# Optimization experiments

Measured on AMD Instinct MI355X. Metric: run time of the kernel, lower is better.

The kernel has to match this reference:

```python
import jax, jax.numpy as jnp
import numpy as np

H, D = 16, 1024
HD = D // H  # 64

def setup_inputs() -> dict:
    key = jax.random.key(0)
    ks = jax.random.split(key, 11)
    B, S = 2, 2048
    s_in = 1.0 / np.sqrt(D)
    return {
        "V": jax.random.normal(ks[0], (B, S, D), jnp.float32),
        "K": jax.random.normal(ks[1], (B, S, D), jnp.float32),
        "Q": jax.random.normal(ks[2], (B, S, D), jnp.float32),
        # stacked per-head Linear weights, torch layout [out,in] -> [H, HD, D]
        "Wv": jax.random.normal(ks[3], (H, HD, D), jnp.float32) * s_in,
        "bv": jnp.zeros((H, HD), jnp.float32),
        "Wk": jax.random.normal(ks[4], (H, HD, D), jnp.float32) * s_in,
        "bk": jnp.zeros((H, HD), jnp.float32),
        "Wq": jax.random.normal(ks[5], (H, HD, D), jnp.float32) * s_in,
        "bq": jnp.zeros((H, HD), jnp.float32),
        "Wo": jax.random.normal(ks[6], (D, D), jnp.float32) * s_in,
        "bo": jnp.zeros((D,), jnp.float32),
    }

def reference(V, K, Q, Wv, bv, Wk, bk, Wq, bq, Wo, bo):
    scale = HD ** (-0.5)
    # per-head projections fused into one batched GEMM: [B,S,D] x [H,HD,D] -> [B,H,S,HD]
    q = jnp.einsum('bsd,hed->bhse', Q, Wq) + bq[None, :, None, :]
    k = jnp.einsum('bsd,hed->bhse', K, Wk) + bk[None, :, None, :]
    v = jnp.einsum('bsd,hed->bhse', V, Wv) + bv[None, :, None, :]
    # scaled dot-product attention
    scores = jnp.einsum('bhqe,bhke->bhqk', q, k) * scale  # [B,H,S,S]
    p = jax.nn.softmax(scores, axis=-1)
    att = jnp.einsum('bhqk,bhke->bhqe', p, v)  # [B,H,S,HD]
    # concat heads (head 0 first, matching the torch cat order) then output proj
    B, _, S, _ = att.shape
    cat = jnp.transpose(att, (0, 2, 1, 3)).reshape(B, S, H * HD)
    return cat @ Wo.T + bo
```

## Files before the change

### kernel.cpp

```cpp
#include <hip/hip_runtime.h>
#include <cstdint>
#include <cstddef>

typedef __bf16 bf16_t;
typedef bf16_t bf16x8 __attribute__((ext_vector_type(8)));
typedef bf16_t bf16x4 __attribute__((ext_vector_type(4)));
typedef float f32x4 __attribute__((ext_vector_type(4)));
typedef float f32x2 __attribute__((ext_vector_type(2)));

__device__ __forceinline__ void gl_lds16(const void* g, void* l) {
  __builtin_amdgcn_global_load_lds(
      (const __attribute__((address_space(1))) void*)g,
      (__attribute__((address_space(3))) void*)l, 16, 0, 0);
}

__device__ __forceinline__ f32x4 mfma16(bf16x8 a, bf16x8 b, f32x4 c) {
  return __builtin_amdgcn_mfma_f32_16x16x32_bf16(a, b, c, 0, 0, 0);
}

__device__ __forceinline__ float exp2_fast(float x) {
  float r;
  asm("v_exp_f32 %0, %1" : "=v"(r) : "v"(x));
  return r;
}

#define SCHED_FENCE() __builtin_amdgcn_sched_barrier(0)
#define WAIT_VM0()   do { asm volatile("s_waitcnt vmcnt(0)");   SCHED_FENCE(); } while (0)
#define WAIT_LGKM0() do { asm volatile("s_waitcnt lgkmcnt(0)"); SCHED_FENCE(); } while (0)
#define RAW_BAR()    do { __builtin_amdgcn_s_barrier();         SCHED_FENCE(); } while (0)

struct CvtArgs { const float* src[7]; bf16_t* dst[7]; };

__global__ __launch_bounds__(256) void convert_all(CvtArgs a) {
  unsigned g = blockIdx.x * 256u + threadIdx.x;
  unsigned seg, off;
  if (g < 524288u) {
    seg = g >> 17; off = g & 131071u;
  } else {
    unsigned h = g - 524288u;
    seg = 4u + (h >> 19); off = h & 524287u;
  }
  const float4* s = (const float4*)a.src[seg] + (size_t)off * 2;
  float4 x0 = s[0], x1 = s[1];
  bf16x8 o;
  o[0] = (bf16_t)x0.x; o[1] = (bf16_t)x0.y; o[2] = (bf16_t)x0.z; o[3] = (bf16_t)x0.w;
  o[4] = (bf16_t)x1.x; o[5] = (bf16_t)x1.y; o[6] = (bf16_t)x1.z; o[7] = (bf16_t)x1.w;
  *(bf16x8*)(a.dst[seg] + (size_t)off * 8) = o;
}

__device__ __forceinline__ void stage128(const bf16_t* src, bf16_t* dst, int t, int w) {
  #pragma unroll
  for (int i = 0; i < 4; i++) {
    int g = t + i * 256;
    int r = g >> 3, pc = g & 7;
    int lc = pc ^ (r & 7);
    gl_lds16(src + (size_t)r * 1024 + lc * 8, dst + i * 2048 + w * 512);
  }
}
__device__ __forceinline__ void stage64(const bf16_t* src, bf16_t* dst, int t, int w) {
  #pragma unroll
  for (int i = 0; i < 2; i++) {
    int g = t + i * 256;
    int r = g >> 3, pc = g & 7;
    int lc = pc ^ (r & 7);
    gl_lds16(src + (size_t)r * 1024 + lc * 8, dst + i * 2048 + w * 512);
  }
}

struct ProjArgs {
  const bf16_t* A[3]; const bf16_t* W[3]; const float* bias[3];
  bf16_t* out[3]; float scale[3];
};

__global__ __launch_bounds__(256, 2) void gemm_proj(ProjArgs p) {
  __shared__ __attribute__((aligned(16))) unsigned char smem[65536];
  const int z = blockIdx.z;
  const bf16_t* A = p.A[z] + (size_t)blockIdx.x * 128 * 1024;
  const bf16_t* W = p.W[z] + (size_t)blockIdx.y * 128 * 1024;

  const int t = threadIdx.x;
  const int w = t >> 6, l = t & 63;
  const int lq = l >> 4, lr = l & 15;
  const int mq = w & 1, nq = w >> 1;

  f32x4 acc[4][4];
  f32x4 zero = {0.f, 0.f, 0.f, 0.f};
  #pragma unroll
  for (int i = 0; i < 4; i++)
    #pragma unroll
    for (int j = 0; j < 4; j++) acc[i][j] = zero;

  stage128(A, (bf16_t*)smem, t, w);
  stage128(W, (bf16_t*)(smem + 16384), t, w);
  WAIT_VM0();
  RAW_BAR();

  for (int step = 0; step < 16; ++step) {
    const int cur = step & 1;
    bf16_t* as = (bf16_t*)(smem + cur * 32768);
    bf16_t* bs = (bf16_t*)(smem + cur * 32768 + 16384);
    if (step < 15) {
      bf16_t* an = (bf16_t*)(smem + (cur ^ 1) * 32768);
      stage128(A + (step + 1) * 64, an, t, w);
      stage128(W + (step + 1) * 64, an + 8192, t, w);
    }
    SCHED_FENCE();
    #pragma unroll
    for (int kk = 0; kk < 2; kk++) {
      bf16x8 af[4], bfr[4];
      #pragma unroll
      for (int i = 0; i < 4; i++) {
        int R = mq * 64 + i * 16 + lr;
        int ch = (kk * 4 + lq) ^ (R & 7);
        af[i] = *(const bf16x8*)(as + R * 64 + ch * 8);
      }
      #pragma unroll
      for (int j = 0; j < 4; j++) {
        int R = nq * 64 + j * 16 + lr;
        int ch = (kk * 4 + lq) ^ (R & 7);
        bfr[j] = *(const bf16x8*)(bs + R * 64 + ch * 8);
      }
      __builtin_amdgcn_s_setprio(1);
      #pragma unroll
      for (int i = 0; i < 4; i++)
        #pragma unroll
        for (int j = 0; j < 4; j++)
          acc[i][j] = mfma16(af[i], bfr[j], acc[i][j]);
      __builtin_amdgcn_s_setprio(0);
    }
    WAIT_VM0();
    RAW_BAR();
  }

  const float* bias = p.bias[z];
  const float scale = p.scale[z];
  __syncthreads();
  bf16_t* ts = (bf16_t*)smem;
  #pragma unroll
  for (int i = 0; i < 4; i++) {
    #pragma unroll
    for (int j = 0; j < 4; j++) {
      int nl = nq * 64 + j * 16 + lr;
      float bz = bias[blockIdx.y * 128 + nl];
      #pragma unroll
      for (int r = 0; r < 4; r++) {
        int ml = mq * 64 + i * 16 + lq * 4 + r;
        bf16_t val = (bf16_t)((acc[i][j][r] + bz) * scale);
        if (z == 0) {
          int mlp = (ml & 96) | (((ml >> 2) & 3) << 3) | (((ml >> 4) & 1) << 2) | (ml & 3);
          ts[nl * 136 + mlp] = val;
        } else {
          ts[ml * 136 + nl] = val;
        }
      }
    }
  }
  __syncthreads();
  bf16_t* out = p.out[z];
  const int b = blockIdx.x >> 4, sbase = (blockIdx.x & 15) * 128;
  if (z == 0) {
    #pragma unroll
    for (int ii = 0; ii < 8; ii++) {
      int idx = t * 8 + ii * 2048;
      int rr = idx >> 7, cc = idx & 127;
      int n = blockIdx.y * 128 + rr;
      int h = n >> 6, e = n & 63;
      bf16x8 vq = *(const bf16x8*)(ts + rr * 136 + cc);
      *(bf16x8*)(out + ((size_t)(b * 16 + h) * 64 + e) * 2048 + sbase + cc) = vq;
    }
  } else {
    #pragma unroll
    for (int ii = 0; ii < 8; ii++) {
      int idx = t * 8 + ii * 2048;
      int rr = idx >> 7, cc = idx & 127;
      int n = blockIdx.y * 128 + cc;
      int h = n >> 6, e = n & 63;
      bf16x8 vq = *(const bf16x8*)(ts + rr * 136 + cc);
      *(bf16x8*)(out + ((size_t)(b * 16 + h) * 2048 + sbase + rr) * 64 + e) = vq;
    }
  }
}

__global__ __launch_bounds__(256, 4) void attn(
    const bf16_t* __restrict__ qw, const bf16_t* __restrict__ kw,
    const bf16_t* __restrict__ vtw, bf16_t* __restrict__ att)
{
  __shared__ __attribute__((aligned(16))) unsigned char smem[32768];
  bf16_t* qe_s = (bf16_t*)(smem + 16384);
  const int bh = blockIdx.x, qt = blockIdx.y;
  const int t = threadIdx.x, w = t >> 6, l = t & 63, lq = l >> 4, lr = l & 15;

  const bf16_t* kb0 = kw + (size_t)bh * 131072;
  const bf16_t* vb0 = vtw + (size_t)bh * 131072;

  const bf16_t* qbase = qw + ((size_t)bh * 2048 + qt * 64) * 64;
  #pragma unroll
  for (int i = 0; i < 2; i++) {
    int g = t + i * 256;
    int r = g >> 3, pc = g & 7;
    int lc = pc ^ (r & 7);
    gl_lds16(qbase + (size_t)r * 64 + lc * 8, qe_s + i * 2048 + w * 512);
    gl_lds16(kb0 + (size_t)r * 64 + lc * 8, (bf16_t*)smem + i * 2048 + w * 512);
    gl_lds16(vb0 + (size_t)r * 2048 + lc * 8, (bf16_t*)(smem + 8192) + i * 2048 + w * 512);
  }
  WAIT_VM0();
  RAW_BAR();
  bf16x8 qf[2];
  #pragma unroll
  for (int kk = 0; kk < 2; kk++) {
    int R = w * 16 + lr;
    int ch = (kk * 4 + lq) ^ (R & 7);
    qf[kk] = *(const bf16x8*)(qe_s + R * 64 + ch * 8);
  }
  WAIT_LGKM0();
  RAW_BAR();

  f32x4 O[4];
  f32x4 zero = {0.f, 0.f, 0.f, 0.f};
  #pragma unroll
  for (int et = 0; et < 4; et++) O[et] = zero;
  f32x2 ls = {0.f, 0.f};
  bf16x8 vf[8];
  bf16x8 pbA[2], pbB[2];

#define ATTN_BODY(KT, CUR, PBOUT, PBIN, FIRST, DOSTAGE)                          \
  {                                                                              \
    bf16_t* ksb = (bf16_t*)(smem + (CUR) * 16384);                               \
    bf16_t* vsb = (bf16_t*)(smem + (CUR) * 16384 + 8192);                        \
    if (DOSTAGE) {                                                               \
      bf16_t* kn = (bf16_t*)(smem + ((CUR) ^ 1) * 16384);                        \
      const bf16_t* kbase = kb0 + (size_t)((KT) + 1) * 4096;                     \
      const bf16_t* vbase = vb0 + (size_t)((KT) + 1) * 64;                       \
      _Pragma("unroll")                                                          \
      for (int i = 0; i < 2; i++) {                                              \
        int g = t + i * 256;                                                     \
        int r = g >> 3, pc = g & 7;                                              \
        int lc = pc ^ (r & 7);                                                   \
        gl_lds16(kbase + (size_t)r * 64 + lc * 8, kn + i * 2048 + w * 512);      \
        gl_lds16(vbase + (size_t)r * 2048 + lc * 8, kn + 4096 + i * 2048 + w * 512); \
      }                                                                          \
    }                                                                            \
    f32x4 sc[4];                                                                 \
    _Pragma("unroll")                                                            \
    for (int j = 0; j < 4; j++) sc[j] = zero;                                    \
    __builtin_amdgcn_s_setprio(1);                                               \
    if (!(FIRST)) {                                                              \
      _Pragma("unroll")                                                          \
      for (int ks2 = 0; ks2 < 2; ks2++)                                          \
        _Pragma("unroll")                                                        \
        for (int et = 0; et < 4; et++)                                           \
          O[et] = mfma16(vf[ks2 * 4 + et], (PBIN)[ks2], O[et]);                  \
    }                                                                            \
    _Pragma("unroll")                                                            \
    for (int kk = 0; kk < 2; kk++)                                               \
      _Pragma("unroll")                                                          \
      for (int j = 0; j < 4; j++) {                                              \
        int R = j * 16 + lr;                                                     \
        int ch = (kk * 4 + lq) ^ (R & 7);                                        \
        bf16x8 kf = *(const bf16x8*)(ksb + R * 64 + ch * 8);                     \
        sc[j] = mfma16(kf, qf[kk], sc[j]);                                       \
      }                                                                          \
    __builtin_amdgcn_s_setprio(0);                                               \
    _Pragma("unroll")                                                            \
    for (int ks2 = 0; ks2 < 2; ks2++)                                            \
      _Pragma("unroll")                                                          \
      for (int et = 0; et < 4; et++) {                                           \
        int R = et * 16 + lr;                                                    \
        int ch = (ks2 * 4 + lq) ^ (R & 7);                                       \
        vf[ks2 * 4 + et] = *(const bf16x8*)(vsb + R * 64 + ch * 8);              \
      }                                                                          \
    _Pragma("unroll")                                                            \
    for (int ks2 = 0; ks2 < 2; ks2++)                                            \
      _Pragma("unroll")                                                          \
      for (int r = 0; r < 4; r++) {                                              \
        float e0 = exp2_fast(sc[2 * ks2][r]);                                    \
        float e1 = exp2_fast(sc[2 * ks2 + 1][r]);                                \
        f32x2 ee = {e0, e1};                                                     \
        ls += ee;                                                                \
        (PBOUT)[ks2][r] = (bf16_t)e0;                                            \
        (PBOUT)[ks2][4 + r] = (bf16_t)e1;                                        \
      }                                                                          \
    WAIT_LGKM0();         \
    if (DOSTAGE) WAIT_VM0();                             \
    RAW_BAR();                                                                   \
  }

  ATTN_BODY(0, 0, pbA, pbB, true, true);
  ATTN_BODY(1, 1, pbB, pbA, false, true);
  for (int kt2 = 1; kt2 < 16; ++kt2) {
    const int kt = kt2 * 2;
    ATTN_BODY(kt, 0, pbA, pbB, false, true);
    ATTN_BODY(kt + 1, 1, pbB, pbA, false, (kt2 < 15));
  }
#undef ATTN_BODY

  #pragma unroll
  for (int ks2 = 0; ks2 < 2; ks2++)
    #pragma unroll
    for (int et = 0; et < 4; et++)
      O[et] = mfma16(vf[ks2 * 4 + et], pbB[ks2], O[et]);

  float s = ls[0] + ls[1];
  s += __shfl_xor(s, 16);
  s += __shfl_xor(s, 32);
  float rinv = 1.0f / s;

  #pragma unroll
  for (int et = 0; et < 4; et++) {
    bf16x4 pv;
    #pragma unroll
    for (int r = 0; r < 4; r++) pv[r] = (bf16_t)(O[et][r] * rinv);
    *(bf16x4*)(qe_s + (w * 16 + lr) * 72 + et * 16 + lq * 4) = pv;
  }
  __syncthreads();
  const int b = bh >> 4, h = bh & 15;
  #pragma unroll
  for (int i = 0; i < 2; i++) {
    int c = t + i * 256;
    int row = c >> 3, c8 = c & 7;
    bf16x8 vv = *(const bf16x8*)(qe_s + row * 72 + c8 * 8);
    *(bf16x8*)(att + ((size_t)b * 2048 + qt * 64 + row) * 1024 + h * 64 + c8 * 8) = vv;
  }
}

__global__ __launch_bounds__(256, 3) void gemm_out(
    const bf16_t* __restrict__ A, const bf16_t* __restrict__ W,
    const float* __restrict__ bias, float* __restrict__ out)
{
  __shared__ __attribute__((aligned(16))) unsigned char smem[49152];
  const bf16_t* Ab = A + (size_t)blockIdx.x * 64 * 1024;
  const bf16_t* Wb = W + (size_t)blockIdx.y * 128 * 1024;
  const int t = threadIdx.x, w = t >> 6, l = t & 63, lq = l >> 4, lr = l & 15;
  const int mh = w & 1, nh = w >> 1;

  f32x4 acc[2][4];
  f32x4 zero = {0.f, 0.f, 0.f, 0.f};
  #pragma unroll
  for (int i = 0; i < 2; i++)
    #pragma unroll
    for (int j = 0; j < 4; j++) acc[i][j] = zero;

  stage64(Ab, (bf16_t*)smem, t, w);
  stage128(Wb, (bf16_t*)(smem + 8192), t, w);
  WAIT_VM0();
  RAW_BAR();

  for (int step = 0; step < 16; ++step) {
    const int cur = step & 1;
    bf16_t* as = (bf16_t*)(smem + cur * 24576);
    bf16_t* bs = (bf16_t*)(smem + cur * 24576 + 8192);
    if (step < 15) {
      bf16_t* an = (bf16_t*)(smem + (cur ^ 1) * 24576);
      stage64(Ab + (step + 1) * 64, an, t, w);
      stage128(Wb + (step + 1) * 64, an + 4096, t, w);
    }
    SCHED_FENCE();
    #pragma unroll
    for (int kk = 0; kk < 2; kk++) {
      bf16x8 af[2], bfr[4];
      #pragma unroll
      for (int i = 0; i < 2; i++) {
        int R = mh * 32 + i * 16 + lr;
        int ch = (kk * 4 + lq) ^ (R & 7);
        af[i] = *(const bf16x8*)(as + R * 64 + ch * 8);
      }
      #pragma unroll
      for (int j = 0; j < 4; j++) {
        int R = nh * 64 + j * 16 + lr;
        int ch = (kk * 4 + lq) ^ (R & 7);
        bfr[j] = *(const bf16x8*)(bs + R * 64 + ch * 8);
      }
      __builtin_amdgcn_s_setprio(1);
      #pragma unroll
      for (int i = 0; i < 2; i++)
        #pragma unroll
        for (int j = 0; j < 4; j++)
          acc[i][j] = mfma16(af[i], bfr[j], acc[i][j]);
      __builtin_amdgcn_s_setprio(0);
    }
    WAIT_VM0();
    RAW_BAR();
  }

  #pragma unroll
  for (int i = 0; i < 2; i++) {
    #pragma unroll
    for (int j = 0; j < 4; j++) {
      int col = blockIdx.y * 128 + nh * 64 + j * 16 + lr;
      float bz = bias[col];
      #pragma unroll
      for (int r = 0; r < 4; r++) {
        int row = blockIdx.x * 64 + mh * 32 + i * 16 + lq * 4 + r;
        out[(size_t)row * 1024 + col] = acc[i][j][r] + bz;
      }
    }
  }
}

extern "C" void kernel_launch(void* const* d_in, const int* in_sizes, int n_in,
                              void* d_out, int out_size, void* d_ws, size_t ws_size,
                              hipStream_t stream) {
  (void)in_sizes; (void)n_in; (void)out_size;
  const float* V  = (const float*)d_in[0];
  const float* Kx = (const float*)d_in[1];
  const float* Q  = (const float*)d_in[2];
  const float* Wv = (const float*)d_in[3];
  const float* bv = (const float*)d_in[4];
  const float* Wk = (const float*)d_in[5];
  const float* bk = (const float*)d_in[6];
  const float* Wq = (const float*)d_in[7];
  const float* bq = (const float*)d_in[8];
  const float* Wo = (const float*)d_in[9];
  const float* bo = (const float*)d_in[10];

  const size_t E = 1048576;
  if (ws_size < 20 * E * sizeof(bf16_t)) return;

  bf16_t* ws = (bf16_t*)d_ws;
  bf16_t* cWo   = ws;
  bf16_t* cWv   = ws + E;
  bf16_t* cWk   = ws + 2 * E;
  bf16_t* cWq   = ws + 3 * E;
  bf16_t* q_ws  = ws + 4 * E;
  bf16_t* k_ws  = ws + 8 * E;
  bf16_t* vt_ws = ws + 12 * E;
  bf16_t* att_ws= ws + 16 * E;

  bf16_t* cV = att_ws;
  bf16_t* cK = (bf16_t*)d_out;
  bf16_t* cQ = (bf16_t*)d_out + 4 * E;

  CvtArgs ca;
  ca.src[0] = Wo; ca.src[1] = Wv; ca.src[2] = Wk; ca.src[3] = Wq;
  ca.src[4] = V;  ca.src[5] = Kx; ca.src[6] = Q;
  ca.dst[0] = cWo; ca.dst[1] = cWv; ca.dst[2] = cWk; ca.dst[3] = cWq;
  ca.dst[4] = cV;  ca.dst[5] = cK;  ca.dst[6] = cQ;
  convert_all<<<8192, 256, 0, stream>>>(ca);

  ProjArgs pa;
  pa.A[0] = cV;  pa.A[1] = cK;  pa.A[2] = cQ;
  pa.W[0] = cWv; pa.W[1] = cWk; pa.W[2] = cWq;
  pa.bias[0] = bv; pa.bias[1] = bk; pa.bias[2] = bq;
  pa.out[0] = vt_ws; pa.out[1] = k_ws; pa.out[2] = q_ws;
  pa.scale[0] = 1.f; pa.scale[1] = 1.f; pa.scale[2] = 0.125f * 1.4426950408889634f;
  gemm_proj<<<dim3(32, 8, 3), 256, 0, stream>>>(pa);

  attn<<<dim3(32, 32), 256, 0, stream>>>(q_ws, k_ws, vt_ws, att_ws);

  gemm_out<<<dim3(64, 8), 256, 0, stream>>>(att_ws, cWo, bo, (float*)d_out);
}
```

Measured before the change: 205.4 us.

## Process 128 query rows per attention block to reuse K/V tiles

Each attention block now handles 128 query rows (two 16-row groups per wave) instead of 64, so each K/V tile staged in LDS feeds twice as many MFMAs. The grid is halved and launch bounds are relaxed to allow more registers for the doubled accumulators and probability fragments. This lowers global and LDS traffic per unit of work, at the cost of higher register pressure, lower occupancy and fewer blocks to spread across CUs.

```diff
diff --git a/kernel.cpp b/kernel.cpp
--- a/kernel.cpp
+++ b/kernel.cpp
@@ -181,47 +181,58 @@
   }
 }
 
-__global__ __launch_bounds__(256, 4) void attn(
+__global__ __launch_bounds__(256, 2) void attn(
     const bf16_t* __restrict__ qw, const bf16_t* __restrict__ kw,
     const bf16_t* __restrict__ vtw, bf16_t* __restrict__ att)
 {
   __shared__ __attribute__((aligned(16))) unsigned char smem[32768];
-  bf16_t* qe_s = (bf16_t*)(smem + 16384);
   const int bh = blockIdx.x, qt = blockIdx.y;
   const int t = threadIdx.x, w = t >> 6, l = t & 63, lq = l >> 4, lr = l & 15;
 
   const bf16_t* kb0 = kw + (size_t)bh * 131072;
   const bf16_t* vb0 = vtw + (size_t)bh * 131072;
-
-  const bf16_t* qbase = qw + ((size_t)bh * 2048 + qt * 64) * 64;
+  bf16_t* qstage = (bf16_t*)(smem + 16384);
+
+  const bf16_t* qbase = qw + ((size_t)bh * 2048 + qt * 128) * 64;
+  #pragma unroll
+  for (int i = 0; i < 4; i++) {
+    int g = t + i * 256;
+    int r = g >> 3, pc = g & 7;
+    int lc = pc ^ (r & 7);
+    gl_lds16(qbase + (size_t)r * 64 + lc * 8, qstage + i * 2048 + w * 512);
+  }
   #pragma unroll
   for (int i = 0; i < 2; i++) {
     int g = t + i * 256;
     int r = g >> 3, pc = g & 7;
     int lc = pc ^ (r & 7);
-    gl_lds16(qbase + (size_t)r * 64 + lc * 8, qe_s + i * 2048 + w * 512);
     gl_lds16(kb0 + (size_t)r * 64 + lc * 8, (bf16_t*)smem + i * 2048 + w * 512);
     gl_lds16(vb0 + (size_t)r * 2048 + lc * 8, (bf16_t*)(smem + 8192) + i * 2048 + w * 512);
   }
   WAIT_VM0();
   RAW_BAR();
-  bf16x8 qf[2];
-  #pragma unroll
-  for (int kk = 0; kk < 2; kk++) {
-    int R = w * 16 + lr;
-    int ch = (kk * 4 + lq) ^ (R & 7);
-    qf[kk] = *(const bf16x8*)(qe_s + R * 64 + ch * 8);
-  }
+  bf16x8 qf[2][2];
+  #pragma unroll
+  for (int gq = 0; gq < 2; gq++)
+    #pragma unroll
+    for (int kk = 0; kk < 2; kk++) {
+      int R = w * 32 + gq * 16 + lr;
+      int ch = (kk * 4 + lq) ^ (R & 7);
+      qf[gq][kk] = *(const bf16x8*)(qstage + R * 64 + ch * 8);
+    }
   WAIT_LGKM0();
   RAW_BAR();
 
-  f32x4 O[4];
+  f32x4 O[2][4];
   f32x4 zero = {0.f, 0.f, 0.f, 0.f};
   #pragma unroll
-  for (int et = 0; et < 4; et++) O[et] = zero;
-  f32x2 ls = {0.f, 0.f};
+  for (int gq = 0; gq < 2; gq++)
+    #pragma unroll
+    for (int et = 0; et < 4; et++) O[gq][et] = zero;
+  f32x2 lsv[2];
+  lsv[0] = f32x2{0.f, 0.f}; lsv[1] = f32x2{0.f, 0.f};
   bf16x8 vf[8];
-  bf16x8 pbA[2], pbB[2];
+  bf16x8 pbA[2][2], pbB[2][2];
 
 #define ATTN_BODY(KT, CUR, PBOUT, PBIN, FIRST, DOSTAGE)                          \
   {                                                                              \
@@ -240,16 +251,20 @@
         gl_lds16(vbase + (size_t)r * 2048 + lc * 8, kn + 4096 + i * 2048 + w * 512); \
       }                                                                          \
     }                                                                            \
-    f32x4 sc[4];                                                                 \
+    f32x4 sc[2][4];                                                              \
     _Pragma("unroll")                                                            \
-    for (int j = 0; j < 4; j++) sc[j] = zero;                                    \
+    for (int gq = 0; gq < 2; gq++)                                               \
+      _Pragma("unroll")                                                          \
+      for (int j = 0; j < 4; j++) sc[gq][j] = zero;                              \
     __builtin_amdgcn_s_setprio(1);                                               \
     if (!(FIRST)) {                                                              \
       _Pragma("unroll")                                                          \
       for (int ks2 = 0; ks2 < 2; ks2++)                                          \
         _Pragma("unroll")                                                        \
-        for (int et = 0; et < 4; et++)                                           \
-          O[et] = mfma16(vf[ks2 * 4 + et], (PBIN)[ks2], O[et]);                  \
+        for (int et = 0; et < 4; et++) {                                         \
+          O[0][et] = mfma16(vf[ks2 * 4 + et], (PBIN)[0][ks2], O[0][et]);         \
+          O[1][et] = mfma16(vf[ks2 * 4 + et], (PBIN)[1][ks2], O[1][et]);         \
+        }                                                                        \
     }                                                                            \
     _Pragma("unroll")                                                            \
     for (int kk = 0; kk < 2; kk++)                                               \
@@ -258,7 +273,8 @@
         int R = j * 16 + lr;                                                     \
         int ch = (kk * 4 + lq) ^ (R & 7);                                        \
         bf16x8 kf = *(const bf16x8*)(ksb + R * 64 + ch * 8);                     \
-        sc[j] = mfma16(kf, qf[kk], sc[j]);                                       \
+        sc[0][j] = mfma16(kf, qf[0][kk], sc[0][j]);                              \
+        sc[1][j] = mfma16(kf, qf[1][kk], sc[1][j]);                              \
       }                                                                          \
     __builtin_amdgcn_s_setprio(0);                                               \
     _Pragma("unroll")                                                            \
@@ -270,16 +286,18 @@
         vf[ks2 * 4 + et] = *(const bf16x8*)(vsb + R * 64 + ch * 8);              \
       }                                                                          \
     _Pragma("unroll")                                                            \
-    for (int ks2 = 0; ks2 < 2; ks2++)                                            \
-      _Pragma("unroll")                                                          \
-      for (int r = 0; r < 4; r++) {                                              \
-        float e0 = exp2_fast(sc[2 * ks2][r]);                                    \
-        float e1 = exp2_fast(sc[2 * ks2 + 1][r]);                                \
-        f32x2 ee = {e0, e1};                                                     \
-        ls += ee;                                                                \
-        (PBOUT)[ks2][r] = (bf16_t)e0;                                            \
-        (PBOUT)[ks2][4 + r] = (bf16_t)e1;                                        \
-      }                                                                          \
+    for (int gq = 0; gq < 2; gq++)                                               \
+      _Pragma("unroll")                                                          \
+      for (int ks2 = 0; ks2 < 2; ks2++)                                          \
+        _Pragma("unroll")                                                        \
+        for (int r = 0; r < 4; r++) {                                            \
+          float e0 = exp2_fast(sc[gq][2 * ks2][r]);                              \
+          float e1 = exp2_fast(sc[gq][2 * ks2 + 1][r]);                          \
+          f32x2 ee = {e0, e1};                                                   \
+          lsv[gq] += ee;                                                         \
+          (PBOUT)[gq][ks2][r] = (bf16_t)e0;                                      \
+          (PBOUT)[gq][ks2][4 + r] = (bf16_t)e1;                                  \
+        }                                                                        \
     WAIT_LGKM0();         \
     if (DOSTAGE) WAIT_VM0();                             \
     RAW_BAR();                                                                   \
@@ -297,29 +315,37 @@
   #pragma unroll
   for (int ks2 = 0; ks2 < 2; ks2++)
     #pragma unroll
-    for (int et = 0; et < 4; et++)
-      O[et] = mfma16(vf[ks2 * 4 + et], pbB[ks2], O[et]);
-
-  float s = ls[0] + ls[1];
-  s += __shfl_xor(s, 16);
-  s += __shfl_xor(s, 32);
-  float rinv = 1.0f / s;
-
-  #pragma unroll
-  for (int et = 0; et < 4; et++) {
-    bf16x4 pv;
-    #pragma unroll
-    for (int r = 0; r < 4; r++) pv[r] = (bf16_t)(O[et][r] * rinv);
-    *(bf16x4*)(qe_s + (w * 16 + lr) * 72 + et * 16 + lq * 4) = pv;
-  }
+    for (int et = 0; et < 4; et++) {
+      O[0][et] = mfma16(vf[ks2 * 4 + et], pbB[0][ks2], O[0][et]);
+      O[1][et] = mfma16(vf[ks2 * 4 + et], pbB[1][ks2], O[1][et]);
+    }
+
+  float s0 = lsv[0][0] + lsv[0][1];
+  float s1 = lsv[1][0] + lsv[1][1];
+  s0 += __shfl_xor(s0, 16);
+  s0 += __shfl_xor(s0, 32);
+  s1 += __shfl_xor(s1, 16);
+  s1 += __shfl_xor(s1, 32);
+  float rinv[2] = {1.0f / s0, 1.0f / s1};
+
+  bf16_t* ts = (bf16_t*)smem;
+  #pragma unroll
+  for (int gq = 0; gq < 2; gq++)
+    #pragma unroll
+    for (int et = 0; et < 4; et++) {
+      bf16x4 pv;
+      #pragma unroll
+      for (int r = 0; r < 4; r++) pv[r] = (bf16_t)(O[gq][et][r] * rinv[gq]);
+      *(bf16x4*)(ts + (w * 32 + gq * 16 + lr) * 72 + et * 16 + lq * 4) = pv;
+    }
   __syncthreads();
   const int b = bh >> 4, h = bh & 15;
   #pragma unroll
-  for (int i = 0; i < 2; i++) {
+  for (int i = 0; i < 4; i++) {
     int c = t + i * 256;
     int row = c >> 3, c8 = c & 7;
-    bf16x8 vv = *(const bf16x8*)(qe_s + row * 72 + c8 * 8);
-    *(bf16x8*)(att + ((size_t)b * 2048 + qt * 64 + row) * 1024 + h * 64 + c8 * 8) = vv;
+    bf16x8 vv = *(const bf16x8*)(ts + row * 72 + c8 * 8);
+    *(bf16x8*)(att + ((size_t)b * 2048 + qt * 128 + row) * 1024 + h * 64 + c8 * 8) = vv;
   }
 }
 
@@ -445,7 +471,7 @@
   pa.scale[0] = 1.f; pa.scale[1] = 1.f; pa.scale[2] = 0.125f * 1.4426950408889634f;
   gemm_proj<<<dim3(32, 8, 3), 256, 0, stream>>>(pa);
 
-  attn<<<dim3(32, 32), 256, 0, stream>>>(q_ws, k_ws, vt_ws, att_ws);
+  attn<<<dim3(32, 16), 256, 0, stream>>>(q_ws, k_ws, vt_ws, att_ws);
 
   gemm_out<<<dim3(64, 8), 256, 0, stream>>>(att_ws, cWo, bo, (float*)d_out);
 }
```

Result: no change. 205.4 us (-0.0%).
